# Kernel optimization log

Hardware: AMD Instinct MI355X
Metric: run time of the kernel (lower is better)

The kernel has to match this reference:

```python
import jax, jax.numpy as jnp
import numpy as np


def setup_inputs() -> dict:
    key = jax.random.key(0)
    k1, k2, k3 = jax.random.split(key, 3)
    B, C, H, Wd = 16, 768, 64, 64
    E = 16
    x = jax.random.normal(k1, (B, C, H, Wd), dtype=jnp.float32)
    # 1x1 conv weight [E, C] (Conv2d weight squeezed) and bias [E]
    W = jax.random.normal(k2, (E, C), dtype=jnp.float32) * (1.0 / np.sqrt(C))
    b = jax.random.normal(k3, (E,), dtype=jnp.float32) * 0.01
    return {"x": x, "W": W, "b": b, "active_experts": 2}


def reference(x, W, b, active_experts):
    # 1x1 conv == pointwise matmul over channel dim: [B,C,H,W] x [E,C] -> [B,E,H,W]
    logits = jnp.einsum("bchw,ec->behw", x, W) + b[None, :, None, None]
    scores = jax.nn.softmax(logits, axis=1)  # softmax over experts
    # top-k along expert axis: move E to last, take top-k, move back
    scores_last = jnp.moveaxis(scores, 1, -1)               # [B,H,W,E]
    topk_probs, topk_indices = jax.lax.top_k(scores_last, active_experts)  # [B,H,W,k]
    topk_probs = topk_probs / jnp.sum(topk_probs, axis=-1, keepdims=True)
    topk_probs = jnp.moveaxis(topk_probs, -1, 1)            # [B,k,H,W]
    topk_indices = jnp.moveaxis(topk_indices, -1, 1)        # [B,k,H,W]
    return topk_probs, topk_indices, scores
```

## Files before the change

### kernel.cpp

```cpp
#include <hip/hip_runtime.h>


#define C_DIM 768
#define E_DIM 16
#define HW    4096
#define NPIX  65536

__global__ __launch_bounds__(256) void transpose_w(
    const float* __restrict__ Wm, float* __restrict__ Wt)
{
    const int t = blockIdx.x * 256 + threadIdx.x;
    if (t < C_DIM * E_DIM) {
        const int c = t >> 4, e = t & 15;
        Wt[t] = Wm[e * C_DIM + c];
    }
}

__global__ __launch_bounds__(256) void router_main(
    const float* __restrict__ x,
    const float* __restrict__ Wt,
    const float* __restrict__ bias,
    float* __restrict__ out)
{
    __shared__ float lds[4][128][17];

    const int p0  = blockIdx.x * 128;
    const int b   = p0 >> 12;
    const int pb  = p0 & 4095;
    const int cg  = __builtin_amdgcn_readfirstlane(threadIdx.x >> 6);
    const int px2 = threadIdx.x & 63;
    const int c0  = cg * 192;

    const float* xp = x + (size_t)b * C_DIM * HW + pb + 2 * px2;

    float2 acc[E_DIM];
#pragma unroll
    for (int e = 0; e < E_DIM; ++e) acc[e] = make_float2(0.f, 0.f);

#pragma unroll 4
    for (int c = c0; c < c0 + 192; ++c) {
        const float2 xv = *reinterpret_cast<const float2*>(xp + (size_t)c * HW);
        const float4* wt = reinterpret_cast<const float4*>(Wt + c * E_DIM);
        const float4 w0 = wt[0], w1 = wt[1], w2 = wt[2], w3 = wt[3];
        acc[ 0].x = fmaf(xv.x, w0.x, acc[ 0].x); acc[ 0].y = fmaf(xv.y, w0.x, acc[ 0].y);
        acc[ 1].x = fmaf(xv.x, w0.y, acc[ 1].x); acc[ 1].y = fmaf(xv.y, w0.y, acc[ 1].y);
        acc[ 2].x = fmaf(xv.x, w0.z, acc[ 2].x); acc[ 2].y = fmaf(xv.y, w0.z, acc[ 2].y);
        acc[ 3].x = fmaf(xv.x, w0.w, acc[ 3].x); acc[ 3].y = fmaf(xv.y, w0.w, acc[ 3].y);
        acc[ 4].x = fmaf(xv.x, w1.x, acc[ 4].x); acc[ 4].y = fmaf(xv.y, w1.x, acc[ 4].y);
        acc[ 5].x = fmaf(xv.x, w1.y, acc[ 5].x); acc[ 5].y = fmaf(xv.y, w1.y, acc[ 5].y);
        acc[ 6].x = fmaf(xv.x, w1.z, acc[ 6].x); acc[ 6].y = fmaf(xv.y, w1.z, acc[ 6].y);
        acc[ 7].x = fmaf(xv.x, w1.w, acc[ 7].x); acc[ 7].y = fmaf(xv.y, w1.w, acc[ 7].y);
        acc[ 8].x = fmaf(xv.x, w2.x, acc[ 8].x); acc[ 8].y = fmaf(xv.y, w2.x, acc[ 8].y);
        acc[ 9].x = fmaf(xv.x, w2.y, acc[ 9].x); acc[ 9].y = fmaf(xv.y, w2.y, acc[ 9].y);
        acc[10].x = fmaf(xv.x, w2.z, acc[10].x); acc[10].y = fmaf(xv.y, w2.z, acc[10].y);
        acc[11].x = fmaf(xv.x, w2.w, acc[11].x); acc[11].y = fmaf(xv.y, w2.w, acc[11].y);
        acc[12].x = fmaf(xv.x, w3.x, acc[12].x); acc[12].y = fmaf(xv.y, w3.x, acc[12].y);
        acc[13].x = fmaf(xv.x, w3.y, acc[13].x); acc[13].y = fmaf(xv.y, w3.y, acc[13].y);
        acc[14].x = fmaf(xv.x, w3.z, acc[14].x); acc[14].y = fmaf(xv.y, w3.z, acc[14].y);
        acc[15].x = fmaf(xv.x, w3.w, acc[15].x); acc[15].y = fmaf(xv.y, w3.w, acc[15].y);
    }

#pragma unroll
    for (int e = 0; e < E_DIM; ++e) {
        lds[cg][2 * px2][e]     = acc[e].x;
        lds[cg][2 * px2 + 1][e] = acc[e].y;
    }
    __syncthreads();

    const int t = threadIdx.x;
    if (t < 128) {
        const int p = pb + t;

        float lg[E_DIM];
#pragma unroll
        for (int e = 0; e < E_DIM; ++e)
            lg[e] = bias[e] + lds[0][t][e] + lds[1][t][e] + lds[2][t][e] + lds[3][t][e];

        float m = -INFINITY;
#pragma unroll
        for (int e = 0; e < E_DIM; ++e) m = fmaxf(m, lg[e]);
        float pr[E_DIM];
        float sum = 0.0f;
#pragma unroll
        for (int e = 0; e < E_DIM; ++e) {
            pr[e] = __expf(lg[e] - m);
            sum += pr[e];
        }
        const float inv = 1.0f / sum;

        float* scores = out + 262144;
#pragma unroll
        for (int e = 0; e < E_DIM; ++e) {
            const float s = pr[e] * inv;
            pr[e] = s;
            scores[(size_t)(b * E_DIM + e) * HW + p] = s;
        }

        int i1 = 0;
        float p1 = pr[0];
#pragma unroll
        for (int e = 1; e < E_DIM; ++e)
            if (pr[e] > p1) { p1 = pr[e]; i1 = e; }
        int i2 = -1;
        float p2 = -INFINITY;
#pragma unroll
        for (int e = 0; e < E_DIM; ++e)
            if (e != i1 && pr[e] > p2) { p2 = pr[e]; i2 = e; }

        const float rs = 1.0f / (p1 + p2);
        const size_t o1 = (size_t)(b * 2 + 0) * HW + p;
        const size_t o2 = (size_t)(b * 2 + 1) * HW + p;
        out[o1] = p1 * rs;
        out[o2] = p2 * rs;
        float* idxo = out + 131072;
        idxo[o1] = (float)i1;
        idxo[o2] = (float)i2;
    }
}

__global__ __launch_bounds__(256) void topk_router_fused(
    const float* __restrict__ x, const float* __restrict__ Wm,
    const float* __restrict__ bias, float* __restrict__ out)
{
    const int g = blockIdx.x * 256 + threadIdx.x;
    const int b = g >> 12;
    const int p = g & 4095;
    const float* xp = x + (size_t)b * C_DIM * HW + p;

    float acc[E_DIM];
#pragma unroll
    for (int e = 0; e < E_DIM; ++e) acc[e] = 0.0f;
#pragma unroll 16
    for (int c = 0; c < C_DIM; ++c) {
        const float xv = xp[(size_t)c * HW];
#pragma unroll
        for (int e = 0; e < E_DIM; ++e)
            acc[e] = fmaf(xv, Wm[e * C_DIM + c], acc[e]);
    }
    float m = -INFINITY;
#pragma unroll
    for (int e = 0; e < E_DIM; ++e) { acc[e] += bias[e]; m = fmaxf(m, acc[e]); }
    float pr[E_DIM]; float sum = 0.0f;
#pragma unroll
    for (int e = 0; e < E_DIM; ++e) { pr[e] = __expf(acc[e] - m); sum += pr[e]; }
    const float inv = 1.0f / sum;
    float* scores = out + 262144;
#pragma unroll
    for (int e = 0; e < E_DIM; ++e) {
        const float s = pr[e] * inv; pr[e] = s;
        scores[(size_t)(b * E_DIM + e) * HW + p] = s;
    }
    int i1 = 0; float p1 = pr[0];
#pragma unroll
    for (int e = 1; e < E_DIM; ++e) if (pr[e] > p1) { p1 = pr[e]; i1 = e; }
    int i2 = -1; float p2 = -INFINITY;
#pragma unroll
    for (int e = 0; e < E_DIM; ++e) if (e != i1 && pr[e] > p2) { p2 = pr[e]; i2 = e; }
    const float rs = 1.0f / (p1 + p2);
    const size_t o1 = (size_t)(b * 2 + 0) * HW + p;
    const size_t o2 = (size_t)(b * 2 + 1) * HW + p;
    out[o1] = p1 * rs; out[o2] = p2 * rs;
    float* idxo = out + 131072;
    idxo[o1] = (float)i1; idxo[o2] = (float)i2;
}

extern "C" void kernel_launch(void* const* d_in, const int* in_sizes, int n_in,
                              void* d_out, int out_size, void* d_ws, size_t ws_size,
                              hipStream_t stream) {
    const float* x  = (const float*)d_in[0];
    const float* Wm = (const float*)d_in[1];
    const float* bs = (const float*)d_in[2];
    float* out = (float*)d_out;
    float* Wt  = (float*)d_ws;

    if (ws_size >= (size_t)C_DIM * E_DIM * sizeof(float)) {
        transpose_w<<<48, 256, 0, stream>>>(Wm, Wt);
        router_main<<<NPIX / 128, 256, 0, stream>>>(x, Wt, bs, out);
    } else {
        topk_router_fused<<<NPIX / 256, 256, 0, stream>>>(x, Wm, bs, out);
    }
}
```

Baseline: 41.32 us.

## Fuse weight transpose into router kernel via LDS staging and serialized reduction

Removes the separate transpose kernel launch. Each block now loads and transposes the full 768x16 weight matrix into shared memory, and the inner loop reads weights from LDS instead of global memory. The cross-wave reduction reuses a single 128x17 buffer, with the four channel groups accumulating in turn under extra barriers. This saves a launch and the workspace dependency, at the cost of 48KB+ of LDS per block, which may cut occupancy, plus a redundant weight load in every block.

```diff
diff --git a/kernel.cpp b/kernel.cpp
--- a/kernel.cpp
+++ b/kernel.cpp
@@ -6,23 +6,25 @@
 #define HW    4096
 #define NPIX  65536
 
-__global__ __launch_bounds__(256) void transpose_w(
-    const float* __restrict__ Wm, float* __restrict__ Wt)
-{
-    const int t = blockIdx.x * 256 + threadIdx.x;
-    if (t < C_DIM * E_DIM) {
-        const int c = t >> 4, e = t & 15;
-        Wt[t] = Wm[e * C_DIM + c];
-    }
-}
-
-__global__ __launch_bounds__(256) void router_main(
+__global__ __launch_bounds__(256) void router_fused(
     const float* __restrict__ x,
-    const float* __restrict__ Wt,
+    const float* __restrict__ Wm,
     const float* __restrict__ bias,
     float* __restrict__ out)
 {
-    __shared__ float lds[4][128][17];
+    __shared__ float wt[C_DIM][E_DIM];
+    __shared__ float red[128][17];
+
+    {
+        const int e  = threadIdx.x & 15;
+        const int cb = threadIdx.x >> 4;
+#pragma unroll
+        for (int j = 0; j < 48; ++j) {
+            const int c = cb + (j << 4);
+            wt[c][e] = Wm[e * C_DIM + c];
+        }
+    }
+    __syncthreads();
 
     const int p0  = blockIdx.x * 128;
     const int b   = p0 >> 12;
@@ -40,8 +42,8 @@
 #pragma unroll 4
     for (int c = c0; c < c0 + 192; ++c) {
         const float2 xv = *reinterpret_cast<const float2*>(xp + (size_t)c * HW);
-        const float4* wt = reinterpret_cast<const float4*>(Wt + c * E_DIM);
-        const float4 w0 = wt[0], w1 = wt[1], w2 = wt[2], w3 = wt[3];
+        const float4* wr = reinterpret_cast<const float4*>(&wt[c][0]);
+        const float4 w0 = wr[0], w1 = wr[1], w2 = wr[2], w3 = wr[3];
         acc[ 0].x = fmaf(xv.x, w0.x, acc[ 0].x); acc[ 0].y = fmaf(xv.y, w0.x, acc[ 0].y);
         acc[ 1].x = fmaf(xv.x, w0.y, acc[ 1].x); acc[ 1].y = fmaf(xv.y, w0.y, acc[ 1].y);
         acc[ 2].x = fmaf(xv.x, w0.z, acc[ 2].x); acc[ 2].y = fmaf(xv.y, w0.z, acc[ 2].y);
@@ -60,12 +62,26 @@
         acc[15].x = fmaf(xv.x, w3.w, acc[15].x); acc[15].y = fmaf(xv.y, w3.w, acc[15].y);
     }
 
+    __syncthreads();
 #pragma unroll
-    for (int e = 0; e < E_DIM; ++e) {
-        lds[cg][2 * px2][e]     = acc[e].x;
-        lds[cg][2 * px2 + 1][e] = acc[e].y;
+    for (int s = 0; s < 4; ++s) {
+        if (cg == s) {
+            if (s == 0) {
+#pragma unroll
+                for (int e = 0; e < E_DIM; ++e) {
+                    red[2 * px2][e]     = acc[e].x;
+                    red[2 * px2 + 1][e] = acc[e].y;
+                }
+            } else {
+#pragma unroll
+                for (int e = 0; e < E_DIM; ++e) {
+                    red[2 * px2][e]     += acc[e].x;
+                    red[2 * px2 + 1][e] += acc[e].y;
+                }
+            }
+        }
+        __syncthreads();
     }
-    __syncthreads();
 
     const int t = threadIdx.x;
     if (t < 128) {
@@ -73,8 +89,7 @@
 
         float lg[E_DIM];
 #pragma unroll
-        for (int e = 0; e < E_DIM; ++e)
-            lg[e] = bias[e] + lds[0][t][e] + lds[1][t][e] + lds[2][t][e] + lds[3][t][e];
+        for (int e = 0; e < E_DIM; ++e) lg[e] = bias[e] + red[t][e];
 
         float m = -INFINITY;
 #pragma unroll
@@ -118,52 +133,6 @@
     }
 }
 
-__global__ __launch_bounds__(256) void topk_router_fused(
-    const float* __restrict__ x, const float* __restrict__ Wm,
-    const float* __restrict__ bias, float* __restrict__ out)
-{
-    const int g = blockIdx.x * 256 + threadIdx.x;
-    const int b = g >> 12;
-    const int p = g & 4095;
-    const float* xp = x + (size_t)b * C_DIM * HW + p;
-
-    float acc[E_DIM];
-#pragma unroll
-    for (int e = 0; e < E_DIM; ++e) acc[e] = 0.0f;
-#pragma unroll 16
-    for (int c = 0; c < C_DIM; ++c) {
-        const float xv = xp[(size_t)c * HW];
-#pragma unroll
-        for (int e = 0; e < E_DIM; ++e)
-            acc[e] = fmaf(xv, Wm[e * C_DIM + c], acc[e]);
-    }
-    float m = -INFINITY;
-#pragma unroll
-    for (int e = 0; e < E_DIM; ++e) { acc[e] += bias[e]; m = fmaxf(m, acc[e]); }
-    float pr[E_DIM]; float sum = 0.0f;
-#pragma unroll
-    for (int e = 0; e < E_DIM; ++e) { pr[e] = __expf(acc[e] - m); sum += pr[e]; }
-    const float inv = 1.0f / sum;
-    float* scores = out + 262144;
-#pragma unroll
-    for (int e = 0; e < E_DIM; ++e) {
-        const float s = pr[e] * inv; pr[e] = s;
-        scores[(size_t)(b * E_DIM + e) * HW + p] = s;
-    }
-    int i1 = 0; float p1 = pr[0];
-#pragma unroll
-    for (int e = 1; e < E_DIM; ++e) if (pr[e] > p1) { p1 = pr[e]; i1 = e; }
-    int i2 = -1; float p2 = -INFINITY;
-#pragma unroll
-    for (int e = 0; e < E_DIM; ++e) if (e != i1 && pr[e] > p2) { p2 = pr[e]; i2 = e; }
-    const float rs = 1.0f / (p1 + p2);
-    const size_t o1 = (size_t)(b * 2 + 0) * HW + p;
-    const size_t o2 = (size_t)(b * 2 + 1) * HW + p;
-    out[o1] = p1 * rs; out[o2] = p2 * rs;
-    float* idxo = out + 131072;
-    idxo[o1] = (float)i1; idxo[o2] = (float)i2;
-}
-
 extern "C" void kernel_launch(void* const* d_in, const int* in_sizes, int n_in,
                               void* d_out, int out_size, void* d_ws, size_t ws_size,
                               hipStream_t stream) {
@@ -171,12 +140,6 @@
     const float* Wm = (const float*)d_in[1];
     const float* bs = (const float*)d_in[2];
     float* out = (float*)d_out;
-    float* Wt  = (float*)d_ws;
 
-    if (ws_size >= (size_t)C_DIM * E_DIM * sizeof(float)) {
-        transpose_w<<<48, 256, 0, stream>>>(Wm, Wt);
-        router_main<<<NPIX / 128, 256, 0, stream>>>(x, Wt, bs, out);
-    } else {
-        topk_router_fused<<<NPIX / 256, 256, 0, stream>>>(x, Wm, bs, out);
-    }
+    router_fused<<<NPIX / 128, 256, 0, stream>>>(x, Wm, bs, out);
 }
```

Result: slower. 48.13 us (+16.5%).
